# Optimization experiments

Measured on AMD Instinct MI355X. Metric: run time of the kernel, lower is better.

The kernel has to match this reference:

```python
import jax, jax.numpy as jnp
import numpy as np

H, E, V, MAXLEN, PAD = 8, 256, 1024, 64, 0


def _ln(x, g, b, eps):
    m = jnp.mean(x, -1, keepdims=True)
    v = jnp.mean((x - m) ** 2, -1, keepdims=True)
    return (x - m) / jnp.sqrt(v + eps) * g + b


def _get_pos(max_len, emb_dim):
    # replicates SVTISDPA.get_pos (sinusoidal, freq built via cumprod)
    half = emb_dim // 2
    freq = jnp.full((half,), 10000.0 ** (-1.0 / half), dtype=jnp.float32).at[0].set(1.0)
    freq = jnp.cumprod(freq)
    phase = jnp.arange(max_len, dtype=jnp.float32)[:, None] * freq[None, :]
    pe = jnp.zeros((max_len, emb_dim), dtype=jnp.float32)
    pe = pe.at[:, 0::2].set(jnp.sin(phase)).at[:, 1::2].set(jnp.cos(phase))
    return pe


def setup_inputs() -> dict:
    key = jax.random.key(0)
    ks = jax.random.split(key, 4)
    char_code = jax.random.randint(ks[0], (512, 64), 0, V)  # [B, max_len]
    emb_w = (jax.random.normal(ks[1], (V, E), dtype=jnp.float32) * 0.05).at[PAD].set(0.0)
    qkv_w = jax.random.normal(ks[2], (3 * E * H, E), dtype=jnp.float32) * 0.05
    fc_w = jax.random.normal(ks[3], (E, E * H), dtype=jnp.float32) * 0.05
    return {
        'char_code': char_code,
        'emb_w': emb_w,
        'qkv_w': qkv_w,
        'fc_w': fc_w,
        'fc_b': jnp.zeros((E,), jnp.float32),
        'sdpa_ln_g': jnp.ones((E,), jnp.float32),
        'sdpa_ln_b': jnp.zeros((E,), jnp.float32),
        'ff_ln_g': jnp.ones((E,), jnp.float32),
        'ff_ln_b': jnp.zeros((E,), jnp.float32),
        'bn_g': jnp.ones((E,), jnp.float32),
        'bn_b': jnp.zeros((E,), jnp.float32),
        'max_len': 64,
    }


def reference(char_code, emb_w, qkv_w, fc_w, fc_b, sdpa_ln_g, sdpa_ln_b,
              ff_ln_g, ff_ln_b, bn_g, bn_b, max_len):
    temp = E ** 0.5
    pos = _get_pos(MAXLEN, E)

    def qkv(x):
        y = (x @ qkv_w.T).reshape(x.shape[0], H, 3 * E)
        return y[..., :E], y[..., E:2 * E], y[..., 2 * E:]

    cq, ck, cv = qkv(emb_w)   # each [V, H, E]
    pq, pk, pv = qkv(pos)     # each [L, H, E]

    char_qk = jnp.einsum('vhe,whe->hvw', cq, ck) / temp          # [H,V,V]
    char_qk = char_qk.at[:, :, PAD].set(-1e9)
    pos_qk = jnp.einsum('lhe,mhe->hlm', pq, pk) / temp           # [H,L,L]
    char_pos_qk = (jnp.einsum('vhe,lhe->hvl', cq, pk)
                   + jnp.einsum('lhe,vhe->hvl', pq, ck)) / temp  # [H,V,L]

    c = char_code[:, :max_len]  # [B,M]
    M = max_len
    # sim[b,h,i,j] = char_qk[h,c_bi,c_bj] + char_pos_qk[h,c_bi,j] + pos_qk[h,i,j]
    sim = (char_qk[:, c[:, :, None], c[:, None, :]]
           + char_pos_qk[:, c, :M]).transpose(1, 0, 2, 3) \
          + pos_qk[None, :, :M, :M]                              # [B,H,M,M]
    attn = jax.nn.softmax(sim, axis=-1)

    not_mask = (c != PAD).astype(sim.dtype)                      # [B,M]
    n_words = jnp.sum(not_mask, -1)                              # [B]
    pooled = jnp.einsum('bm,bhmj->bhj', not_mask, attn) / n_words[:, None, None]

    v = cv[c].transpose(0, 2, 1, 3) + pv.transpose(1, 0, 2)[None, :, :M]  # [B,H,M,E]
    out = jnp.einsum('bhm,bhme->bhe', pooled, v).reshape(c.shape[0], H * E)
    out = _ln(out @ fc_w.T + fc_b, sdpa_ln_g, sdpa_ln_b, 1e-5)
    # FeedForward.forward returns layer_norm(x) (residual branch is dead code)
    out = _ln(out, ff_ln_g, ff_ln_b, 1e-6) + out
    return _ln(out, bn_g, bn_b, 1e-5)
```

## Files before the change

### kernel.cpp

```cpp
#include <hip/hip_runtime.h>
#include <math.h>

typedef unsigned short u16;
typedef __attribute__((ext_vector_type(4))) float f32x4;
typedef __attribute__((ext_vector_type(8))) short s16x8;
typedef __attribute__((ext_vector_type(4))) unsigned short u16x4;
typedef __attribute__((ext_vector_type(8))) unsigned short u16x8;

__device__ __forceinline__ u16 f2b(float f) {
  union { float f; unsigned u; } v; v.f = f;
  return (u16)((v.u + 0x7fffu + ((v.u >> 16) & 1u)) >> 16);
}
__device__ __forceinline__ float b2f(u16 b) {
  union { unsigned u; float f; } v; v.u = ((unsigned)b) << 16;
  return v.f;
}

__global__ __launch_bounds__(256) void prep_kernel(
    const float* __restrict__ emb, const float* __restrict__ qkv,
    const float* __restrict__ fc,
    u16* __restrict__ emb_bf, u16* __restrict__ qkvw_bf, u16* __restrict__ fcx,
    u16* __restrict__ pe)
{
  const int bid = blockIdx.x;
  if (bid < 2304) {
    const int i = bid * 256 + threadIdx.x;
    if (i < 65536) {
      f32x4 v = *(const f32x4*)&emb[(size_t)i * 4];
      u16x4 o = { f2b(v[0]), f2b(v[1]), f2b(v[2]), f2b(v[3]) };
      *(u16x4*)&emb_bf[(size_t)i * 4] = o;
    } else if (i < 458752) {
      const int off = i - 65536;
      f32x4 v = *(const f32x4*)&qkv[(size_t)off * 4];
      u16x4 o = { f2b(v[0]), f2b(v[1]), f2b(v[2]), f2b(v[3]) };
      *(u16x4*)&qkvw_bf[(size_t)off * 4] = o;
    } else {
      const int off4 = (i - 458752) * 4;
      const int row = off4 >> 11, col = off4 & 2047;
      f32x4 v = *(const f32x4*)&fc[(size_t)off4];
      u16x4 o = { f2b(v[0]), f2b(v[1]), f2b(v[2]), f2b(v[3]) };
      *(u16x4*)&fcx[(size_t)row * 2560 + col] = o;
    }
  } else {
    const int t = threadIdx.x;
    const int m = (bid - 2304) * 2 + (t >> 7);
    const int k = t & 127;
    double f = pow(10000.0, -(double)k / 128.0);
    float ph = (float)m * (float)f;
    pe[m * 256 + 2 * k]     = f2b(sinf(ph));
    pe[m * 256 + 2 * k + 1] = f2b(cosf(ph));
  }
}

__global__ __launch_bounds__(256) void gemm128(
    const u16* __restrict__ A, int lda,
    const u16* __restrict__ B, int ldb,
    u16* __restrict__ C, int ldc, int K)
{
  __shared__ __align__(16) u16 As[128 * 64];
  __shared__ __align__(16) u16 Bs[128 * 64];
  const int m0 = blockIdx.y * 128, n0 = blockIdx.x * 128;
  const int tid = threadIdx.x;
  const int w = tid >> 6, l = tid & 63, hi = l >> 4, lo = l & 15;
  const int wr = (w >> 1) * 64, wc = (w & 1) * 64;
  const int srow = tid >> 3, scol = (tid & 7) * 8;
  f32x4 acc[4][4] = {};
  for (int k0 = 0; k0 < K; k0 += 64) {
    __syncthreads();
    #pragma unroll
    for (int q = 0; q < 4; ++q) {
      const int row = q * 32 + srow;
      const int sidx = row * 64 + (scol ^ ((row & 7) << 3));
      *(u16x8*)&As[sidx] = *(const u16x8*)&A[(long)(m0 + row) * lda + k0 + scol];
      *(u16x8*)&Bs[sidx] = *(const u16x8*)&B[(long)(n0 + row) * ldb + k0 + scol];
    }
    __syncthreads();
    #pragma unroll
    for (int kk = 0; kk < 2; ++kk) {
      s16x8 a[4], bf[4];
      #pragma unroll
      for (int m = 0; m < 4; ++m) {
        const int ar = wr + m * 16 + lo;
        a[m] = *(const s16x8*)&As[ar * 64 + ((hi * 8 + kk * 32) ^ ((ar & 7) << 3))];
      }
      #pragma unroll
      for (int n = 0; n < 4; ++n) {
        const int br = wc + n * 16 + lo;
        bf[n] = *(const s16x8*)&Bs[br * 64 + ((hi * 8 + kk * 32) ^ ((br & 7) << 3))];
      }
      #pragma unroll
      for (int m = 0; m < 4; ++m)
        #pragma unroll
        for (int n = 0; n < 4; ++n)
          acc[m][n] = __builtin_amdgcn_mfma_f32_16x16x32_bf16(a[m], bf[n], acc[m][n], 0, 0, 0);
    }
  }
  #pragma unroll
  for (int m = 0; m < 4; ++m)
    #pragma unroll
    for (int n = 0; n < 4; ++n)
      #pragma unroll
      for (int r = 0; r < 4; ++r)
        C[(long)(m0 + wr + m * 16 + hi * 4 + r) * ldc + n0 + wc + n * 16 + lo] = f2b(acc[m][n][r]);
}

template<bool CBF16, bool BIAS>
__global__ __launch_bounds__(256) void gemm_bf(
    const u16* __restrict__ A, int lda, long sA,
    const u16* __restrict__ B, int ldb, long sB,
    void* __restrict__ Cv, int ldc, long sC,
    const float* __restrict__ bias, int K)
{
  __shared__ __align__(16) u16 As[64 * 64];
  __shared__ __align__(16) u16 Bs[64 * 64];
  const int z = blockIdx.z;
  A += (long)z * sA;  B += (long)z * sB;
  const int m0 = blockIdx.y * 64, n0 = blockIdx.x * 64;
  const int tid = threadIdx.x;
  const int srow = tid >> 2, sq = tid & 3;
  const int w = tid >> 6, l = tid & 63, hi = l >> 4, lo = l & 15;
  f32x4 acc[4] = {};
  for (int k0 = 0; k0 < K; k0 += 64) {
    __syncthreads();
    #pragma unroll
    for (int p = 0; p < 2; ++p) {
      const int col = sq * 16 + p * 8;
      const int sidx = srow * 64 + (col ^ ((srow & 7) << 3));
      *(u16x8*)&As[sidx] = *(const u16x8*)&A[(long)(m0 + srow) * lda + k0 + col];
      *(u16x8*)&Bs[sidx] = *(const u16x8*)&B[(long)(n0 + srow) * ldb + k0 + col];
    }
    __syncthreads();
    #pragma unroll
    for (int kk = 0; kk < 2; ++kk) {
      const int arow = w * 16 + lo;
      s16x8 a = *(const s16x8*)&As[arow * 64 + ((hi * 8 + kk * 32) ^ ((arow & 7) << 3))];
      #pragma unroll
      for (int n = 0; n < 4; ++n) {
        const int brow = n * 16 + lo;
        s16x8 bfr = *(const s16x8*)&Bs[brow * 64 + ((hi * 8 + kk * 32) ^ ((brow & 7) << 3))];
        acc[n] = __builtin_amdgcn_mfma_f32_16x16x32_bf16(a, bfr, acc[n], 0, 0, 0);
      }
    }
  }
  const long zoff = (long)z * sC;
  #pragma unroll
  for (int n = 0; n < 4; ++n) {
    #pragma unroll
    for (int r = 0; r < 4; ++r) {
      const int row = m0 + w * 16 + hi * 4 + r;
      const int col = n0 + n * 16 + lo;
      if (CBF16) {
        ((u16*)Cv)[zoff + (long)row * ldc + col] = f2b(acc[n][r]);
      } else {
        float* C = (float*)Cv;
        float v = acc[n][r];
        if (BIAS)  v += bias[col];
        C[zoff + (long)row * ldc + col] = v;
      }
    }
  }
}

__global__ __launch_bounds__(256) void gemm_cpqk(
    const u16* __restrict__ cqkv, const u16* __restrict__ pqkv,
    u16* __restrict__ C)
{
  __shared__ __align__(16) u16 As1[64 * 64], As2[64 * 64];
  __shared__ __align__(16) u16 Bs1[64 * 64], Bs2[64 * 64];
  const int h = blockIdx.z;
  const long hq = (long)h * 768;
  const int m0 = blockIdx.y * 64;
  const int tid = threadIdx.x;
  const int srow = tid >> 2, sq = tid & 3;
  const int w = tid >> 6, l = tid & 63, hi = l >> 4, lo = l & 15;
  f32x4 acc[4] = {};
  for (int k0 = 0; k0 < 256; k0 += 64) {
    __syncthreads();
    #pragma unroll
    for (int p = 0; p < 2; ++p) {
      const int col = sq * 16 + p * 8;
      const int sidx = srow * 64 + (col ^ ((srow & 7) << 3));
      const long arow = (long)(m0 + srow) * 6144 + hq + k0 + col;
      const long brow = (long)srow * 6144 + hq + k0 + col;
      *(u16x8*)&As1[sidx] = *(const u16x8*)&cqkv[arow + 256];
      *(u16x8*)&As2[sidx] = *(const u16x8*)&cqkv[arow];
      *(u16x8*)&Bs1[sidx] = *(const u16x8*)&pqkv[brow];
      *(u16x8*)&Bs2[sidx] = *(const u16x8*)&pqkv[brow + 256];
    }
    __syncthreads();
    #pragma unroll
    for (int kk = 0; kk < 2; ++kk) {
      const int arow = w * 16 + lo;
      const int aidx = arow * 64 + ((hi * 8 + kk * 32) ^ ((arow & 7) << 3));
      s16x8 a1 = *(const s16x8*)&As1[aidx];
      s16x8 a2 = *(const s16x8*)&As2[aidx];
      #pragma unroll
      for (int n = 0; n < 4; ++n) {
        const int brow = n * 16 + lo;
        const int bidx = brow * 64 + ((hi * 8 + kk * 32) ^ ((brow & 7) << 3));
        acc[n] = __builtin_amdgcn_mfma_f32_16x16x32_bf16(a1, *(const s16x8*)&Bs1[bidx], acc[n], 0, 0, 0);
        acc[n] = __builtin_amdgcn_mfma_f32_16x16x32_bf16(a2, *(const s16x8*)&Bs2[bidx], acc[n], 0, 0, 0);
      }
    }
  }
  #pragma unroll
  for (int n = 0; n < 4; ++n)
    #pragma unroll
    for (int r = 0; r < 4; ++r)
      C[(long)h * 65536 + (long)(m0 + w * 16 + hi * 4 + r) * 64 + n * 16 + lo] = f2b(acc[n][r]);
}

__global__ __launch_bounds__(256, 4) void attn_kernel(
    const int* __restrict__ cc, const u16* __restrict__ cqkv,
    const u16* __restrict__ cpqk, const u16* __restrict__ pqk,
    u16* __restrict__ outp)
{
  __shared__ __align__(16) u16 Ks[64 * 256];
  __shared__ int   cs[64];
  __shared__ float notm[64];
  __shared__ float poolp[4][64];
  __shared__ float pooled[64];
  __shared__ float nwords;
  const int h = blockIdx.x, b = blockIdx.y;
  const int tid = threadIdx.x;
  const long hq = (long)h * 768;

  if (tid < 64) {
    const int c = cc[b * 64 + tid];
    cs[tid] = c;
    notm[tid] = c ? 1.f : 0.f;
    unsigned long long bm = __ballot(c != 0);
    if (tid == 0) nwords = (float)__popcll(bm);
  }
  __syncthreads();

  const int srow = tid >> 2, sq = tid & 3;
  const int w = tid >> 6, l = tid & 63, hi = l >> 4, lo = l & 15;
  const int swz = (srow & 7) << 3;
  const int ci_s = cs[srow];

  const long crow = ((long)h * 1024 + ci_s) * 64;
  const long prow = (long)h * 4096 + (long)srow * 64;
  u16x8 ct0 = *(const u16x8*)&cpqk[crow + sq * 8];
  u16x8 ct1 = *(const u16x8*)&cpqk[crow + sq * 8 + 32];
  u16x8 pt0 = *(const u16x8*)&pqk[prow + sq * 8];
  u16x8 pt1 = *(const u16x8*)&pqk[prow + sq * 8 + 32];

  const long qrow = (long)cs[w * 16 + lo] * 6144 + hq;
  s16x8 a[8];
  #pragma unroll
  for (int kk = 0; kk < 8; ++kk)
    a[kk] = *(const s16x8*)&cqkv[qrow + kk * 32 + hi * 8];

  {
    const long kbase = (long)ci_s * 6144 + hq + 256;
    u16x8 kr[8];
    #pragma unroll
    for (int p = 0; p < 8; ++p)
      kr[p] = *(const u16x8*)&cqkv[kbase + sq * 8 + p * 32];
    #pragma unroll
    for (int p = 0; p < 8; ++p)
      *(u16x8*)&Ks[srow * 256 + ((sq * 8 + p * 32) ^ swz)] = kr[p];
  }

  const long vrow = (long)ci_s * 6144 + hq + 512;
  u16x8 va[8];
  #pragma unroll
  for (int p = 0; p < 8; ++p)
    va[p] = *(const u16x8*)&cqkv[vrow + sq * 8 + p * 32];

  __syncthreads();

  f32x4 acc[4] = {};
  #pragma unroll
  for (int kk = 0; kk < 8; ++kk) {
    #pragma unroll
    for (int n = 0; n < 4; ++n) {
      const int brow = n * 16 + lo;
      s16x8 bfr = *(const s16x8*)&Ks[brow * 256 + ((hi * 8 + kk * 32) ^ ((brow & 7) << 3))];
      acc[n] = __builtin_amdgcn_mfma_f32_16x16x32_bf16(a[kk], bfr, acc[n], 0, 0, 0);
    }
  }
  __syncthreads();

  *(u16x8*)&Ks[srow * 64 + ((sq * 8) ^ swz)]          = ct0;
  *(u16x8*)&Ks[srow * 64 + ((sq * 8 + 32) ^ swz)]     = ct1;
  *(u16x8*)&Ks[4096 + srow * 64 + ((sq * 8) ^ swz)]      = pt0;
  *(u16x8*)&Ks[4096 + srow * 64 + ((sq * 8 + 32) ^ swz)] = pt1;
  __syncthreads();

  const float scale = 0.0625f;
  int csj[4];
  #pragma unroll
  for (int n = 0; n < 4; ++n) csj[n] = cs[n * 16 + lo];
  float ex[4][4];
  float wgt[4];
  #pragma unroll
  for (int r = 0; r < 4; ++r) {
    const int i = w * 16 + hi * 4 + r;
    const int tswz = (i & 7) << 3;
    float s[4];
    float mx = -3e38f;
    #pragma unroll
    for (int n = 0; n < 4; ++n) {
      const int j = n * 16 + lo;
      const int cidx = i * 64 + (j ^ tswz);
      float v = (acc[n][r] + b2f(Ks[cidx]) + b2f(Ks[4096 + cidx])) * scale;
      if (csj[n] == 0) v = -1e9f;
      s[n] = v;
      mx = fmaxf(mx, v);
    }
    mx = fmaxf(mx, __shfl_xor(mx, 1));
    mx = fmaxf(mx, __shfl_xor(mx, 2));
    mx = fmaxf(mx, __shfl_xor(mx, 4));
    mx = fmaxf(mx, __shfl_xor(mx, 8));
    float sum = 0.f;
    #pragma unroll
    for (int n = 0; n < 4; ++n) { const float e = __expf(s[n] - mx); ex[n][r] = e; sum += e; }
    sum += __shfl_xor(sum, 1);
    sum += __shfl_xor(sum, 2);
    sum += __shfl_xor(sum, 4);
    sum += __shfl_xor(sum, 8);
    wgt[r] = notm[i] / sum;
  }
  #pragma unroll
  for (int n = 0; n < 4; ++n) {
    float cp = ex[n][0] * wgt[0] + ex[n][1] * wgt[1] + ex[n][2] * wgt[2] + ex[n][3] * wgt[3];
    cp += __shfl_xor(cp, 16);
    cp += __shfl_xor(cp, 32);
    if (hi == 0) poolp[w][n * 16 + lo] = cp;
  }
  __syncthreads();

  float pval = 0.f;
  if (tid < 64) {
    pval = (poolp[0][tid] + poolp[1][tid] + poolp[2][tid] + poolp[3][tid]) / nwords;
    pooled[tid] = pval;
  }

  #pragma unroll
  for (int p = 0; p < 8; ++p)
    *(u16x8*)&Ks[srow * 256 + ((sq * 8 + p * 32) ^ swz)] = va[p];

  if (tid < 64)
    outp[(long)b * 2560 + 2048 + h * 64 + tid] = f2b(pval);
  __syncthreads();

  float o = 0.f;
  #pragma unroll
  for (int j = 0; j < 64; ++j)
    o += pooled[j] * b2f(Ks[j * 256 + (tid ^ ((j & 7) << 3))]);
  outp[(long)b * 2560 + h * 256 + tid] = f2b(o);
}

__global__ __launch_bounds__(256) void ln_chain(
    const float* __restrict__ xp, const float* __restrict__ fcb,
    const float* __restrict__ g1, const float* __restrict__ b1,
    const float* __restrict__ g2, const float* __restrict__ b2,
    const float* __restrict__ g3, const float* __restrict__ b3,
    float* __restrict__ out)
{
  __shared__ float red[4];
  const int b = blockIdx.x, t = threadIdx.x;
  const long idx = (long)b * 256 + t;
  float v = xp[idx] + xp[idx + 131072] + xp[idx + 262144] + xp[idx + 393216] + fcb[t];

  auto bsum = [&](float val) -> float {
    #pragma unroll
    for (int o = 32; o; o >>= 1) val += __shfl_down(val, o);
    __syncthreads();
    if ((t & 63) == 0) red[t >> 6] = val;
    __syncthreads();
    return red[0] + red[1] + red[2] + red[3];
  };

  float mean = bsum(v) * (1.f / 256.f);
  float d = v - mean;
  float var = bsum(d * d) * (1.f / 256.f);
  const float y1 = d * rsqrtf(var + 1e-5f) * g1[t] + b1[t];

  mean = bsum(y1) * (1.f / 256.f);
  d = y1 - mean;
  var = bsum(d * d) * (1.f / 256.f);
  const float y2 = d * rsqrtf(var + 1e-6f) * g2[t] + b2[t] + y1;

  mean = bsum(y2) * (1.f / 256.f);
  d = y2 - mean;
  var = bsum(d * d) * (1.f / 256.f);
  out[idx] = d * rsqrtf(var + 1e-5f) * g3[t] + b3[t];
}

extern "C" void kernel_launch(void* const* d_in, const int* in_sizes, int n_in,
                              void* d_out, int out_size, void* d_ws, size_t ws_size,
                              hipStream_t stream) {
  (void)in_sizes; (void)n_in; (void)out_size; (void)ws_size;
  const int*   cc    = (const int*)  d_in[0];
  const float* emb_w = (const float*)d_in[1];
  const float* qkv_w = (const float*)d_in[2];
  const float* fc_w  = (const float*)d_in[3];
  const float* fc_b  = (const float*)d_in[4];
  const float* sg    = (const float*)d_in[5];
  const float* sb    = (const float*)d_in[6];
  const float* fg    = (const float*)d_in[7];
  const float* fb    = (const float*)d_in[8];
  const float* bg    = (const float*)d_in[9];
  const float* bbv   = (const float*)d_in[10];
  float* out = (float*)d_out;

  char* p = (char*)d_ws;
  u16* pe_bf   = (u16*)p;  p += (size_t)64 * 256 * 2;
  u16* emb_bf  = (u16*)p;  p += (size_t)1024 * 256 * 2;
  u16* qkvw_bf = (u16*)p;  p += (size_t)6144 * 256 * 2;
  u16* fcx     = (u16*)p;  p += (size_t)256 * 2560 * 2;
  u16* cqkv_bf = (u16*)p;  p += (size_t)1024 * 6144 * 2;
  u16* pqkv_bf = (u16*)p;  p += (size_t)64 * 6144 * 2;
  u16* cpqk16  = (u16*)p;  p += (size_t)8 * 1024 * 64 * 2;
  u16* pqk16   = (u16*)p;  p += (size_t)8 * 64 * 64 * 2;
  u16* sdpa_bf = (u16*)p;  p += (size_t)512 * 2560 * 2;
  float* fco   = (float*)p; p += (size_t)4 * 512 * 256 * 4;

  prep_kernel<<<dim3(2336), dim3(256), 0, stream>>>(
      emb_w, qkv_w, fc_w, emb_bf, qkvw_bf, fcx, pe_bf);

  gemm128<<<dim3(48, 8), dim3(256), 0, stream>>>(
      emb_bf, 256, qkvw_bf, 256, cqkv_bf, 6144, 256);
  gemm_bf<true, false><<<dim3(96, 1, 1), dim3(256), 0, stream>>>(
      pe_bf, 256, 0, qkvw_bf, 256, 0, pqkv_bf, 6144, 0, nullptr, 256);
  gemm_cpqk<<<dim3(1, 16, 8), dim3(256), 0, stream>>>(cqkv_bf, pqkv_bf, cpqk16);
  gemm_bf<true, false><<<dim3(1, 1, 8), dim3(256), 0, stream>>>(
      pqkv_bf, 6144, 768, pqkv_bf + 256, 6144, 768, pqk16, 64, 4096, nullptr, 256);
  gemm_bf<true, false><<<dim3(1, 4, 8), dim3(256), 0, stream>>>(
      fcx, 2560, 256, pqkv_bf + 512, 6144, 768, fcx + 2048, 2560, 64, nullptr, 256);

  attn_kernel<<<dim3(8, 512), dim3(256), 0, stream>>>(
      cc, cqkv_bf, cpqk16, pqk16, sdpa_bf);

  gemm_bf<false, false><<<dim3(4, 8, 4), dim3(256), 0, stream>>>(
      sdpa_bf, 2560, 640, fcx, 2560, 640, fco, 256, (long)512 * 256, nullptr, 640);

  ln_chain<<<dim3(512), dim3(256), 0, stream>>>(fco, fc_b, sg, sb, fg, fb, bg, bbv, out);
}
```

Measured before the change: 96.20 us.

## Merge precompute GEMM launches and trim attention kernel shared state

The positional QKV projection is folded into the char QKV GEMM by padding the position table to 128 rows and adding a ninth row of tiles. The three small table GEMMs (char-pos, pos-pos, pos-value x fc) are merged into one heterogeneous launch with per-block dispatch. The attention kernel drops its shared token and mask arrays, reads codes directly, broadcasts pooled weights via shuffles, reuses the K buffer for partial sums, and raises the occupancy hint to 5. This cuts launch count and serialized tiny kernels, in exchange for wasted work on the padded position rows and more register pressure from the higher occupancy hint.

```diff
diff --git a/kernel.cpp b/kernel.cpp
--- a/kernel.cpp
+++ b/kernel.cpp
@@ -45,34 +45,42 @@
     const int t = threadIdx.x;
     const int m = (bid - 2304) * 2 + (t >> 7);
     const int k = t & 127;
-    double f = pow(10000.0, -(double)k / 128.0);
-    float ph = (float)m * (float)f;
-    pe[m * 256 + 2 * k]     = f2b(sinf(ph));
-    pe[m * 256 + 2 * k + 1] = f2b(cosf(ph));
+    float sv = 0.f, cv = 0.f;
+    if (m < 64) {
+      double f = pow(10000.0, -(double)k / 128.0);
+      float ph = (float)m * (float)f;
+      sv = sinf(ph); cv = cosf(ph);
+    }
+    pe[m * 256 + 2 * k]     = f2b(sv);
+    pe[m * 256 + 2 * k + 1] = f2b(cv);
   }
 }
 
 __global__ __launch_bounds__(256) void gemm128(
-    const u16* __restrict__ A, int lda,
-    const u16* __restrict__ B, int ldb,
-    u16* __restrict__ C, int ldc, int K)
+    const u16* __restrict__ emb, const u16* __restrict__ pe,
+    const u16* __restrict__ B,
+    u16* __restrict__ Ccq, u16* __restrict__ Cpq)
 {
   __shared__ __align__(16) u16 As[128 * 64];
   __shared__ __align__(16) u16 Bs[128 * 64];
-  const int m0 = blockIdx.y * 128, n0 = blockIdx.x * 128;
+  const int ytile = blockIdx.y;
+  const u16* A; u16* C; int m0;
+  if (ytile < 8) { A = emb; C = Ccq; m0 = ytile * 128; }
+  else           { A = pe;  C = Cpq; m0 = 0; }
+  const int n0 = blockIdx.x * 128;
   const int tid = threadIdx.x;
   const int w = tid >> 6, l = tid & 63, hi = l >> 4, lo = l & 15;
   const int wr = (w >> 1) * 64, wc = (w & 1) * 64;
   const int srow = tid >> 3, scol = (tid & 7) * 8;
   f32x4 acc[4][4] = {};
-  for (int k0 = 0; k0 < K; k0 += 64) {
+  for (int k0 = 0; k0 < 256; k0 += 64) {
     __syncthreads();
     #pragma unroll
     for (int q = 0; q < 4; ++q) {
       const int row = q * 32 + srow;
       const int sidx = row * 64 + (scol ^ ((row & 7) << 3));
-      *(u16x8*)&As[sidx] = *(const u16x8*)&A[(long)(m0 + row) * lda + k0 + scol];
-      *(u16x8*)&Bs[sidx] = *(const u16x8*)&B[(long)(n0 + row) * ldb + k0 + scol];
+      *(u16x8*)&As[sidx] = *(const u16x8*)&A[(long)(m0 + row) * 256 + k0 + scol];
+      *(u16x8*)&Bs[sidx] = *(const u16x8*)&B[(long)(n0 + row) * 256 + k0 + scol];
     }
     __syncthreads();
     #pragma unroll
@@ -101,15 +109,13 @@
     for (int n = 0; n < 4; ++n)
       #pragma unroll
       for (int r = 0; r < 4; ++r)
-        C[(long)(m0 + wr + m * 16 + hi * 4 + r) * ldc + n0 + wc + n * 16 + lo] = f2b(acc[m][n][r]);
-}
-
-template<bool CBF16, bool BIAS>
+        C[(long)(m0 + wr + m * 16 + hi * 4 + r) * 6144 + n0 + wc + n * 16 + lo] = f2b(acc[m][n][r]);
+}
+
 __global__ __launch_bounds__(256) void gemm_bf(
     const u16* __restrict__ A, int lda, long sA,
     const u16* __restrict__ B, int ldb, long sB,
-    void* __restrict__ Cv, int ldc, long sC,
-    const float* __restrict__ bias, int K)
+    float* __restrict__ C, int ldc, long sC, int K)
 {
   __shared__ __align__(16) u16 As[64 * 64];
   __shared__ __align__(16) u16 Bs[64 * 64];
@@ -144,32 +150,37 @@
   }
   const long zoff = (long)z * sC;
   #pragma unroll
-  for (int n = 0; n < 4; ++n) {
-    #pragma unroll
-    for (int r = 0; r < 4; ++r) {
-      const int row = m0 + w * 16 + hi * 4 + r;
-      const int col = n0 + n * 16 + lo;
-      if (CBF16) {
-        ((u16*)Cv)[zoff + (long)row * ldc + col] = f2b(acc[n][r]);
-      } else {
-        float* C = (float*)Cv;
-        float v = acc[n][r];
-        if (BIAS)  v += bias[col];
-        C[zoff + (long)row * ldc + col] = v;
-      }
-    }
-  }
-}
-
-__global__ __launch_bounds__(256) void gemm_cpqk(
+  for (int n = 0; n < 4; ++n)
+    #pragma unroll
+    for (int r = 0; r < 4; ++r)
+      C[zoff + (long)(m0 + w * 16 + hi * 4 + r) * ldc + n0 + n * 16 + lo] = acc[n][r];
+}
+
+__global__ __launch_bounds__(256) void tables_kernel(
     const u16* __restrict__ cqkv, const u16* __restrict__ pqkv,
-    u16* __restrict__ C)
-{
-  __shared__ __align__(16) u16 As1[64 * 64], As2[64 * 64];
-  __shared__ __align__(16) u16 Bs1[64 * 64], Bs2[64 * 64];
-  const int h = blockIdx.z;
-  const long hq = (long)h * 768;
-  const int m0 = blockIdx.y * 64;
+    const u16* __restrict__ fcx,
+    u16* __restrict__ cpqk, u16* __restrict__ pqk, u16* __restrict__ pvfc)
+{
+  __shared__ __align__(16) u16 As1[64 * 64], Bs1[64 * 64];
+  __shared__ __align__(16) u16 As2[64 * 64], Bs2[64 * 64];
+  const int blk = blockIdx.x;
+  const u16 *A1, *A2 = nullptr, *B1, *B2 = nullptr;
+  u16* C; int lda, ldb, ldc, m0; bool dual = false;
+  if (blk < 128) {
+    const int h = blk & 7, mt = blk >> 3;
+    A1 = cqkv + h * 768 + 256; A2 = cqkv + h * 768;
+    B1 = pqkv + h * 768;       B2 = pqkv + h * 768 + 256;
+    lda = 6144; ldb = 6144; C = cpqk + (long)h * 65536; ldc = 64;
+    m0 = mt * 64; dual = true;
+  } else if (blk < 136) {
+    const int h = blk - 128;
+    A1 = pqkv + h * 768; B1 = pqkv + h * 768 + 256;
+    lda = 6144; ldb = 6144; C = pqk + h * 4096; ldc = 64; m0 = 0;
+  } else {
+    const int idx = blk - 136, h = idx & 7, mt = idx >> 3;
+    A1 = fcx + h * 256; B1 = pqkv + 512 + h * 768;
+    lda = 2560; ldb = 6144; C = pvfc + h * 64; ldc = 2560; m0 = mt * 64;
+  }
   const int tid = threadIdx.x;
   const int srow = tid >> 2, sq = tid & 3;
   const int w = tid >> 6, l = tid & 63, hi = l >> 4, lo = l & 15;
@@ -180,12 +191,12 @@
     for (int p = 0; p < 2; ++p) {
       const int col = sq * 16 + p * 8;
       const int sidx = srow * 64 + (col ^ ((srow & 7) << 3));
-      const long arow = (long)(m0 + srow) * 6144 + hq + k0 + col;
-      const long brow = (long)srow * 6144 + hq + k0 + col;
-      *(u16x8*)&As1[sidx] = *(const u16x8*)&cqkv[arow + 256];
-      *(u16x8*)&As2[sidx] = *(const u16x8*)&cqkv[arow];
-      *(u16x8*)&Bs1[sidx] = *(const u16x8*)&pqkv[brow];
-      *(u16x8*)&Bs2[sidx] = *(const u16x8*)&pqkv[brow + 256];
+      *(u16x8*)&As1[sidx] = *(const u16x8*)&A1[(long)(m0 + srow) * lda + k0 + col];
+      *(u16x8*)&Bs1[sidx] = *(const u16x8*)&B1[(long)srow * ldb + k0 + col];
+      if (dual) {
+        *(u16x8*)&As2[sidx] = *(const u16x8*)&A2[(long)(m0 + srow) * lda + k0 + col];
+        *(u16x8*)&Bs2[sidx] = *(const u16x8*)&B2[(long)srow * ldb + k0 + col];
+      }
     }
     __syncthreads();
     #pragma unroll
@@ -193,13 +204,20 @@
       const int arow = w * 16 + lo;
       const int aidx = arow * 64 + ((hi * 8 + kk * 32) ^ ((arow & 7) << 3));
       s16x8 a1 = *(const s16x8*)&As1[aidx];
-      s16x8 a2 = *(const s16x8*)&As2[aidx];
       #pragma unroll
       for (int n = 0; n < 4; ++n) {
         const int brow = n * 16 + lo;
         const int bidx = brow * 64 + ((hi * 8 + kk * 32) ^ ((brow & 7) << 3));
         acc[n] = __builtin_amdgcn_mfma_f32_16x16x32_bf16(a1, *(const s16x8*)&Bs1[bidx], acc[n], 0, 0, 0);
-        acc[n] = __builtin_amdgcn_mfma_f32_16x16x32_bf16(a2, *(const s16x8*)&Bs2[bidx], acc[n], 0, 0, 0);
+      }
+      if (dual) {
+        s16x8 a2 = *(const s16x8*)&As2[aidx];
+        #pragma unroll
+        for (int n = 0; n < 4; ++n) {
+          const int brow = n * 16 + lo;
+          const int bidx = brow * 64 + ((hi * 8 + kk * 32) ^ ((brow & 7) << 3));
+          acc[n] = __builtin_amdgcn_mfma_f32_16x16x32_bf16(a2, *(const s16x8*)&Bs2[bidx], acc[n], 0, 0, 0);
+        }
       }
     }
   }
@@ -207,37 +225,26 @@
   for (int n = 0; n < 4; ++n)
     #pragma unroll
     for (int r = 0; r < 4; ++r)
-      C[(long)h * 65536 + (long)(m0 + w * 16 + hi * 4 + r) * 64 + n * 16 + lo] = f2b(acc[n][r]);
-}
-
-__global__ __launch_bounds__(256, 4) void attn_kernel(
+      C[(long)(m0 + w * 16 + hi * 4 + r) * ldc + n * 16 + lo] = f2b(acc[n][r]);
+}
+
+__global__ __launch_bounds__(256, 5) void attn_kernel(
     const int* __restrict__ cc, const u16* __restrict__ cqkv,
     const u16* __restrict__ cpqk, const u16* __restrict__ pqk,
     u16* __restrict__ outp)
 {
   __shared__ __align__(16) u16 Ks[64 * 256];
-  __shared__ int   cs[64];
-  __shared__ float notm[64];
-  __shared__ float poolp[4][64];
-  __shared__ float pooled[64];
-  __shared__ float nwords;
   const int h = blockIdx.x, b = blockIdx.y;
   const int tid = threadIdx.x;
   const long hq = (long)h * 768;
-
-  if (tid < 64) {
-    const int c = cc[b * 64 + tid];
-    cs[tid] = c;
-    notm[tid] = c ? 1.f : 0.f;
-    unsigned long long bm = __ballot(c != 0);
-    if (tid == 0) nwords = (float)__popcll(bm);
-  }
-  __syncthreads();
+  const int* ccb = cc + b * 64;
 
   const int srow = tid >> 2, sq = tid & 3;
   const int w = tid >> 6, l = tid & 63, hi = l >> 4, lo = l & 15;
   const int swz = (srow & 7) << 3;
-  const int ci_s = cs[srow];
+
+  const int ci_s = ccb[srow];
+  const float invn = 1.f / (float)__popcll(__ballot(ccb[l] != 0));
 
   const long crow = ((long)h * 1024 + ci_s) * 64;
   const long prow = (long)h * 4096 + (long)srow * 64;
@@ -246,7 +253,7 @@
   u16x8 pt0 = *(const u16x8*)&pqk[prow + sq * 8];
   u16x8 pt1 = *(const u16x8*)&pqk[prow + sq * 8 + 32];
 
-  const long qrow = (long)cs[w * 16 + lo] * 6144 + hq;
+  const long qrow = (long)ccb[w * 16 + lo] * 6144 + hq;
   s16x8 a[8];
   #pragma unroll
   for (int kk = 0; kk < 8; ++kk)
@@ -283,8 +290,8 @@
   }
   __syncthreads();
 
-  *(u16x8*)&Ks[srow * 64 + ((sq * 8) ^ swz)]          = ct0;
-  *(u16x8*)&Ks[srow * 64 + ((sq * 8 + 32) ^ swz)]     = ct1;
+  *(u16x8*)&Ks[srow * 64 + ((sq * 8) ^ swz)]             = ct0;
+  *(u16x8*)&Ks[srow * 64 + ((sq * 8 + 32) ^ swz)]        = ct1;
   *(u16x8*)&Ks[4096 + srow * 64 + ((sq * 8) ^ swz)]      = pt0;
   *(u16x8*)&Ks[4096 + srow * 64 + ((sq * 8 + 32) ^ swz)] = pt1;
   __syncthreads();
@@ -292,7 +299,7 @@
   const float scale = 0.0625f;
   int csj[4];
   #pragma unroll
-  for (int n = 0; n < 4; ++n) csj[n] = cs[n * 16 + lo];
+  for (int n = 0; n < 4; ++n) csj[n] = ccb[n * 16 + lo];
   float ex[4][4];
   float wgt[4];
   #pragma unroll
@@ -321,35 +328,32 @@
     sum += __shfl_xor(sum, 2);
     sum += __shfl_xor(sum, 4);
     sum += __shfl_xor(sum, 8);
-    wgt[r] = notm[i] / sum;
-  }
+    wgt[r] = (ccb[i] != 0 ? 1.f : 0.f) / sum;
+  }
+  float* poolpF = (float*)&Ks[8192];
   #pragma unroll
   for (int n = 0; n < 4; ++n) {
     float cp = ex[n][0] * wgt[0] + ex[n][1] * wgt[1] + ex[n][2] * wgt[2] + ex[n][3] * wgt[3];
     cp += __shfl_xor(cp, 16);
     cp += __shfl_xor(cp, 32);
-    if (hi == 0) poolp[w][n * 16 + lo] = cp;
-  }
-  __syncthreads();
-
-  float pval = 0.f;
-  if (tid < 64) {
-    pval = (poolp[0][tid] + poolp[1][tid] + poolp[2][tid] + poolp[3][tid]) / nwords;
-    pooled[tid] = pval;
-  }
+    if (hi == 0) poolpF[w * 64 + n * 16 + lo] = cp;
+  }
+  __syncthreads();
+
+  const float pl = (poolpF[l] + poolpF[64 + l] + poolpF[128 + l] + poolpF[192 + l]) * invn;
+  if (tid < 64)
+    outp[(long)b * 2560 + 2048 + h * 64 + tid] = f2b(pl);
+  __syncthreads();
 
   #pragma unroll
   for (int p = 0; p < 8; ++p)
     *(u16x8*)&Ks[srow * 256 + ((sq * 8 + p * 32) ^ swz)] = va[p];
-
-  if (tid < 64)
-    outp[(long)b * 2560 + 2048 + h * 64 + tid] = f2b(pval);
   __syncthreads();
 
   float o = 0.f;
   #pragma unroll
   for (int j = 0; j < 64; ++j)
-    o += pooled[j] * b2f(Ks[j * 256 + (tid ^ ((j & 7) << 3))]);
+    o += __shfl(pl, j) * b2f(Ks[j * 256 + (tid ^ ((j & 7) << 3))]);
   outp[(long)b * 2560 + h * 256 + tid] = f2b(o);
 }
 
@@ -408,35 +412,31 @@
   float* out = (float*)d_out;
 
   char* p = (char*)d_ws;
-  u16* pe_bf   = (u16*)p;  p += (size_t)64 * 256 * 2;
+  u16* pe_pad  = (u16*)p;  p += (size_t)128 * 256 * 2;
   u16* emb_bf  = (u16*)p;  p += (size_t)1024 * 256 * 2;
   u16* qkvw_bf = (u16*)p;  p += (size_t)6144 * 256 * 2;
   u16* fcx     = (u16*)p;  p += (size_t)256 * 2560 * 2;
   u16* cqkv_bf = (u16*)p;  p += (size_t)1024 * 6144 * 2;
-  u16* pqkv_bf = (u16*)p;  p += (size_t)64 * 6144 * 2;
+  u16* pqkv_bf = (u16*)p;  p += (size_t)128 * 6144 * 2;
   u16* cpqk16  = (u16*)p;  p += (size_t)8 * 1024 * 64 * 2;
   u16* pqk16   = (u16*)p;  p += (size_t)8 * 64 * 64 * 2;
   u16* sdpa_bf = (u16*)p;  p += (size_t)512 * 2560 * 2;
   float* fco   = (float*)p; p += (size_t)4 * 512 * 256 * 4;
 
-  prep_kernel<<<dim3(2336), dim3(256), 0, stream>>>(
-      emb_w, qkv_w, fc_w, emb_bf, qkvw_bf, fcx, pe_bf);
-
-  gemm128<<<dim3(48, 8), dim3(256), 0, stream>>>(
-      emb_bf, 256, qkvw_bf, 256, cqkv_bf, 6144, 256);
-  gemm_bf<true, false><<<dim3(96, 1, 1), dim3(256), 0, stream>>>(
-      pe_bf, 256, 0, qkvw_bf, 256, 0, pqkv_bf, 6144, 0, nullptr, 256);
-  gemm_cpqk<<<dim3(1, 16, 8), dim3(256), 0, stream>>>(cqkv_bf, pqkv_bf, cpqk16);
-  gemm_bf<true, false><<<dim3(1, 1, 8), dim3(256), 0, stream>>>(
-      pqkv_bf, 6144, 768, pqkv_bf + 256, 6144, 768, pqk16, 64, 4096, nullptr, 256);
-  gemm_bf<true, false><<<dim3(1, 4, 8), dim3(256), 0, stream>>>(
-      fcx, 2560, 256, pqkv_bf + 512, 6144, 768, fcx + 2048, 2560, 64, nullptr, 256);
+  prep_kernel<<<dim3(2368), dim3(256), 0, stream>>>(
+      emb_w, qkv_w, fc_w, emb_bf, qkvw_bf, fcx, pe_pad);
+
+  gemm128<<<dim3(48, 9), dim3(256), 0, stream>>>(
+      emb_bf, pe_pad, qkvw_bf, cqkv_bf, pqkv_bf);
+
+  tables_kernel<<<dim3(168), dim3(256), 0, stream>>>(
+      cqkv_bf, pqkv_bf, fcx, cpqk16, pqk16, fcx + 2048);
 
   attn_kernel<<<dim3(8, 512), dim3(256), 0, stream>>>(
       cc, cqkv_bf, cpqk16, pqk16, sdpa_bf);
 
-  gemm_bf<false, false><<<dim3(4, 8, 4), dim3(256), 0, stream>>>(
-      sdpa_bf, 2560, 640, fcx, 2560, 640, fco, 256, (long)512 * 256, nullptr, 640);
+  gemm_bf<<<dim3(4, 8, 4), dim3(256), 0, stream>>>(
+      sdpa_bf, 2560, 640, fcx, 2560, 640, fco, 256, (long)512 * 256, 640);
 
   ln_chain<<<dim3(512), dim3(256), 0, stream>>>(fco, fc_b, sg, sb, fg, fb, bg, bbv, out);
 }
```

Result: slower. 118.3 us (+23.0%).
